# Performance work log

Hardware: AMD Instinct MI355X
Metric: run time of the kernel (lower is better)

The kernel has to match this reference:

```python
import jax, jax.numpy as jnp
import numpy as np

N = 100000
E = 1600000
EMB = 64
IN = 64
HID = 64
HEADS = 3
NEG_SLOPE = 0.2            # PyG GATConv default LeakyReLU slope
RRELU_SLOPE = (1.0 / 8.0 + 1.0 / 3.0) / 2.0  # torch.rrelu eval-mode slope


def setup_inputs() -> dict:
    key = jax.random.key(0)
    ks = jax.random.split(key, 16)
    d_in = IN + EMB
    inp = {
        "z": jax.random.normal(ks[0], (N, EMB), jnp.float32),
        "x": jax.random.normal(ks[1], (N, IN), jnp.float32),
        "edge_index": jax.random.randint(ks[2], (2, E), 0, N, jnp.int32),
        # gat1: (in+emb) -> hidden, 3 heads, concat=False
        "W1": jax.random.normal(ks[3], (d_in, HEADS * HID), jnp.float32) / np.sqrt(d_in),
        "att_src1": jax.random.normal(ks[4], (HEADS, HID), jnp.float32) / np.sqrt(HID),
        "att_dst1": jax.random.normal(ks[5], (HEADS, HID), jnp.float32) / np.sqrt(HID),
        "bias1": jnp.zeros((HID,), jnp.float32),
        # gat2: hidden -> hidden, 3 heads, concat=True
        "W2": jax.random.normal(ks[6], (HID, HEADS * HID), jnp.float32) / np.sqrt(HID),
        "att_src2": jax.random.normal(ks[7], (HEADS, HID), jnp.float32) / np.sqrt(HID),
        "att_dst2": jax.random.normal(ks[8], (HEADS, HID), jnp.float32) / np.sqrt(HID),
        "bias2": jnp.zeros((HEADS * HID,), jnp.float32),
        # final linear hidden*3 -> 1 (with bias)
        "lin_w": jax.random.normal(ks[9], (HEADS * HID, 1), jnp.float32) / np.sqrt(HEADS * HID),
        "lin_b": jnp.zeros((1,), jnp.float32),
    }
    return inp


def rrelu_eval(x):
    return jnp.where(x >= 0, x, x * RRELU_SLOPE)


def gat_conv(x, src, dst, W, a_src, a_dst, bias, concat):
    """PyG GATConv (shared src/dst projection, self-loops already appended)."""
    n = x.shape[0]
    H, C = a_src.shape
    xl = (x @ W).reshape(n, H, C)                       # [N, H, C]
    s = jnp.einsum('nhc,hc->nh', xl, a_src)             # alpha_src per node
    d = jnp.einsum('nhc,hc->nh', xl, a_dst)             # alpha_dst per node
    alpha = jax.nn.leaky_relu(s[src] + d[dst], NEG_SLOPE)  # [E', H]
    amax = jax.ops.segment_max(alpha, dst, num_segments=n)
    ex = jnp.exp(alpha - amax[dst])
    denom = jax.ops.segment_sum(ex, dst, num_segments=n)
    w = ex / (denom[dst] + 1e-16)                       # segment softmax
    out = jax.ops.segment_sum(xl[src] * w[:, :, None], dst, num_segments=n)  # [N,H,C]
    out = out.reshape(n, H * C) if concat else out.mean(axis=1)
    return out + bias


def reference(z, x, edge_index, W1, att_src1, att_dst1, bias1,
              W2, att_src2, att_dst2, bias2, lin_w, lin_b):
    n = x.shape[0]
    loops = jnp.arange(n, dtype=edge_index.dtype)
    src = jnp.concatenate([edge_index[0], loops])       # add self-loops (PyG default)
    dst = jnp.concatenate([edge_index[1], loops])
    h = jnp.concatenate([z, x], axis=1)
    h = rrelu_eval(gat_conv(h, src, dst, W1, att_src1, att_dst1, bias1, concat=False))
    h = rrelu_eval(gat_conv(h, src, dst, W2, att_src2, att_dst2, bias2, concat=True))
    return h @ lin_w + lin_b
```

## Files before the change

### kernel.cpp

```cpp
#include <hip/hip_runtime.h>
#include <cstdint>
#include <cstddef>

#define NEG_SLOPE 0.2f
#define RRELU_SLOPE 0.22916666666666666f

#define BSHIFT 6
#define BCAP 1536
#define MAXNB 1600

typedef _Float16 half4 __attribute__((ext_vector_type(4)));
typedef _Float16 half8 __attribute__((ext_vector_type(8)));
typedef float f32x4 __attribute__((ext_vector_type(4)));

__device__ __forceinline__ float wave_sum64(float v) {
#pragma unroll
  for (int o = 32; o > 0; o >>= 1) v += __shfl_xor(v, o, 64);
  return v;
}

__global__ __launch_bounds__(256) void bucketA(const int* __restrict__ src,
                                               const int* __restrict__ dst, int E, int NB,
                                               int* __restrict__ cursor,
                                               int* __restrict__ region) {
  __shared__ int hist[MAXNB];
  __shared__ int gbase[MAXNB];
  const int tid = threadIdx.x;
  const int chunk = (E + gridDim.x - 1) / gridDim.x;
  const int e0 = blockIdx.x * chunk;
  const int e1 = min(e0 + chunk, E);
  for (int b = tid; b < NB; b += 256) hist[b] = 0;
  __syncthreads();
  for (int i = e0 + tid; i < e1; i += 256) {
    atomicAdd(&hist[dst[i] >> BSHIFT], 1);
  }
  __syncthreads();
  for (int b = tid; b < NB; b += 256) {
    int c = hist[b];
    gbase[b] = (c > 0) ? atomicAdd(&cursor[b], c) : 0;
    hist[b] = 0;
  }
  __syncthreads();
  for (int i = e0 + tid; i < e1; i += 256) {
    int d = dst[i];
    int b = d >> BSHIFT;
    int idx = atomicAdd(&hist[b], 1) + gbase[b];
    if (idx < BCAP) region[b * BCAP + idx] = src[i] | ((d & 63) << 17);
  }
}

__global__ __launch_bounds__(256) void bucket_scan(const int* __restrict__ cursor, int NB,
                                                   int* __restrict__ colbase) {
  __shared__ int lds[256];
  const int tid = threadIdx.x;
  const int K = (NB + 255) / 256;
  int vals[8];
  int s = 0;
#pragma unroll
  for (int j = 0; j < 8; j++) {
    int b = tid * K + j;
    int v = (j < K && b < NB) ? (min(cursor[b], BCAP) + 64) : 0;
    vals[j] = v;
    s += v;
  }
  lds[tid] = s;
  __syncthreads();
  for (int o = 1; o < 256; o <<= 1) {
    int t = (tid >= o) ? lds[tid - o] : 0;
    __syncthreads();
    lds[tid] += t;
    __syncthreads();
  }
  int off = (tid > 0) ? lds[tid - 1] : 0;
#pragma unroll
  for (int j = 0; j < 8; j++) {
    int b = tid * K + j;
    if (j < K && b < NB) colbase[b] = off;
    off += vals[j];
  }
}

__global__ __launch_bounds__(256) void bucketB(const int* __restrict__ region,
                                               const int* __restrict__ cursor,
                                               const int* __restrict__ colbase, int NB,
                                               int* __restrict__ rp, int* __restrict__ col) {
  __shared__ int lcnt[64];
  __shared__ int loff[64];
  const int b = blockIdx.x;
  const int tid = threadIdx.x;
  const int cnt = min(cursor[b], BCAP);
  const int base = colbase[b];
  if (tid < 64) lcnt[tid] = 0;
  __syncthreads();
  const int* reg = region + (size_t)b * BCAP;
  for (int i = tid; i < cnt; i += 256) {
    atomicAdd(&lcnt[reg[i] >> 17], 1);
  }
  __syncthreads();
  if (tid < 64) {
    int v = lcnt[tid] + 1;
    int inc = v;
#pragma unroll
    for (int o = 1; o < 64; o <<= 1) {
      int t = __shfl_up(inc, o, 64);
      if (tid >= o) inc += t;
    }
    int excl = inc - v;
    loff[tid] = excl;
    int n = (b << BSHIFT) + tid;
    rp[n] = base + excl;
    col[base + excl] = n;
    lcnt[tid] = 1;
  }
  __syncthreads();
  for (int i = tid; i < cnt; i += 256) {
    int r = reg[i];
    int ld = r >> 17;
    int idx = atomicAdd(&lcnt[ld], 1);
    col[base + loff[ld] + idx] = r & 0x1FFFF;
  }
}

#define APAD 72
#define BTPAD 72

template <int KC>
__global__ __launch_bounds__(256, 4) void gemm_sd_kernel(
    const float* __restrict__ A0, const float* __restrict__ A1,
    const float* __restrict__ W, const float* __restrict__ asrc,
    const float* __restrict__ adst, _Float16* __restrict__ xlh,
    float* __restrict__ sdS, float* __restrict__ sdD, int N) {
  __shared__ _Float16 A16[64 * APAD];
  __shared__ _Float16 Bt[192 * BTPAD];
  const int tid = threadIdx.x;
  const int w = tid >> 6;
  const int lane = tid & 63;
  const int m = lane & 15;
  const int q = lane >> 4;
  const int m0 = blockIdx.x * 64;

  f32x4 acc[12];
#pragma unroll
  for (int t = 0; t < 12; t++) acc[t] = (f32x4)(0.f);

  for (int kc = 0; kc < KC; kc++) {
    const float* __restrict__ Ab = (KC == 2 && kc == 1) ? A1 : A0;
    if (kc > 0) __syncthreads();
#pragma unroll
    for (int i = 0; i < 4; i++) {
      int f = tid + 256 * i;
      int row = f >> 4;
      int c4 = f & 15;
      int gr = m0 + row;
      gr = (gr < N) ? gr : (N - 1);
      float4 v = *(const float4*)(Ab + (size_t)gr * 64 + c4 * 4);
      half4 hv;
      hv.x = (_Float16)v.x; hv.y = (_Float16)v.y;
      hv.z = (_Float16)v.z; hv.w = (_Float16)v.w;
      *(half4*)&A16[row * APAD + c4 * 4] = hv;
    }
#pragma unroll
    for (int i = 0; i < 6; i++) {
      int f = tid + 256 * i;
      int kg = f / 192;
      int c = f % 192;
      half8 hv;
#pragma unroll
      for (int j = 0; j < 8; j++) {
        hv[j] = (_Float16)W[(size_t)(kc * 64 + kg * 8 + j) * 192 + c];
      }
      *(half8*)&Bt[c * BTPAD + kg * 8] = hv;
    }
    __syncthreads();

#pragma unroll
    for (int t = 0; t < 2; t++) {
      half8 af = *(const half8*)&A16[(w * 16 + m) * APAD + t * 32 + q * 8];
#pragma unroll
      for (int ct = 0; ct < 12; ct++) {
        half8 bf = *(const half8*)&Bt[(ct * 16 + m) * BTPAD + t * 32 + q * 8];
        acc[ct] = __builtin_amdgcn_mfma_f32_16x16x32_f16(af, bf, acc[ct], 0, 0, 0);
      }
    }
  }

  float avs[12], avd[12];
#pragma unroll
  for (int ct = 0; ct < 12; ct++) {
    avs[ct] = asrc[ct * 16 + m];
    avd[ct] = adst[ct * 16 + m];
  }
#pragma unroll
  for (int r = 0; r < 4; r++) {
    const int gr = m0 + w * 16 + q * 4 + r;
    const bool ok = gr < N;
    if (ok) {
#pragma unroll
      for (int ct = 0; ct < 12; ct++) {
        xlh[(size_t)gr * 192 + ct * 16 + m] = (_Float16)acc[ct][r];
      }
    }
#pragma unroll
    for (int h = 0; h < 3; h++) {
      float ps = acc[h * 4 + 0][r] * avs[h * 4 + 0] + acc[h * 4 + 1][r] * avs[h * 4 + 1] +
                 acc[h * 4 + 2][r] * avs[h * 4 + 2] + acc[h * 4 + 3][r] * avs[h * 4 + 3];
      float pd = acc[h * 4 + 0][r] * avd[h * 4 + 0] + acc[h * 4 + 1][r] * avd[h * 4 + 1] +
                 acc[h * 4 + 2][r] * avd[h * 4 + 2] + acc[h * 4 + 3][r] * avd[h * 4 + 3];
#pragma unroll
      for (int o = 1; o < 16; o <<= 1) {
        ps += __shfl_xor(ps, o, 64);
        pd += __shfl_xor(pd, o, 64);
      }
      if (ok && m == 0) {
        sdS[(size_t)gr * 4 + h] = ps;
        sdD[(size_t)gr * 4 + h] = pd;
      }
    }
  }
}

template <int D>
__device__ __forceinline__ void gather_fma_d(const _Float16* __restrict__ xlh,
                                             const float2* __restrict__ wob, int t,
                                             unsigned laneoff, float* acc) {
  half8 xv[D];
  float wgt[D];
#pragma unroll
  for (int u = 0; u < D; u++) {
    float2 rec = wob[2 * (t + u)];
    unsigned off = __float_as_uint(rec.x) + laneoff;
    wgt[u] = rec.y;
    xv[u] = *(const half8*)((const char*)xlh + off);
  }
#pragma unroll
  for (int u = 0; u < D; u++) {
#pragma unroll
    for (int k = 0; k < 8; k++) acc[k] += (float)xv[u][k] * wgt[u];
  }
}

template <int MODE>
__global__ __launch_bounds__(256) void agg_kernel(
    const _Float16* __restrict__ xlh, const float4* __restrict__ sdS,
    const float4* __restrict__ sdD, const int* __restrict__ rp,
    const int* __restrict__ col, const float* __restrict__ bias,
    const float* __restrict__ lw, const float* __restrict__ lb,
    float* __restrict__ out, int N) {
  __shared__ float2 wo[4][3][64];
  const int lane = threadIdx.x & 63;
  const int wv = threadIdx.x >> 6;
  const int n = blockIdx.x * 4 + wv;
  if (n >= N) return;
  const int beg = rp[n], end = rp[n + 1];
  const float4 dd = sdD[n];
  const int s = lane & 31;
  const int h = (s < 24) ? (s >> 3) : 0;
  const int g = s & 7;
  const int par = lane >> 5;
  const unsigned laneoff = (unsigned)(h * 128 + g * 16);
  const float2* wob = &wo[wv][h][par];

  float l0 = 0.f, l1 = 0.f, l2 = 0.f;
  float acc[8];
#pragma unroll
  for (int k = 0; k < 8; k++) acc[k] = 0.f;

  for (int j0 = beg; j0 < end; j0 += 64) {
    const int cntc = min(64, end - j0);
    const bool valid = lane < cntc;
    int srcv = valid ? col[j0 + lane] : 0;
    float4 s4 = sdS[srcv];
    float t0 = s4.x + dd.x, t1 = s4.y + dd.y, t2 = s4.z + dd.z;
    t0 = (t0 < 0.f) ? t0 * NEG_SLOPE : t0;
    t1 = (t1 < 0.f) ? t1 * NEG_SLOPE : t1;
    t2 = (t2 < 0.f) ? t2 * NEG_SLOPE : t2;
    float e0 = valid ? __expf(t0) : 0.f;
    float e1 = valid ? __expf(t1) : 0.f;
    float e2 = valid ? __expf(t2) : 0.f;
    l0 += e0; l1 += e1; l2 += e2;
    const float offb = __uint_as_float((unsigned)srcv * 384u);
    wo[wv][0][lane] = make_float2(offb, e0);
    wo[wv][1][lane] = make_float2(offb, e1);
    wo[wv][2][lane] = make_float2(offb, e2);
    const int steps = (cntc + 1) >> 1;
    int t = 0;
    for (; t + 6 <= steps; t += 6) {
      gather_fma_d<6>(xlh, wob, t, laneoff, acc);
    }
    if (t + 3 <= steps) {
      gather_fma_d<3>(xlh, wob, t, laneoff, acc);
      t += 3;
    }
    if (t + 2 <= steps) {
      gather_fma_d<2>(xlh, wob, t, laneoff, acc);
      t += 2;
    }
    if (t < steps) {
      gather_fma_d<1>(xlh, wob, t, laneoff, acc);
    }
  }

#pragma unroll
  for (int k = 0; k < 8; k++) acc[k] += __shfl_xor(acc[k], 32, 64);
  l0 = wave_sum64(l0);
  l1 = wave_sum64(l1);
  l2 = wave_sum64(l2);
  const float invl = 1.0f / (((h == 0) ? l0 : ((h == 1) ? l1 : l2)) + 1e-16f);
  float v[8];
#pragma unroll
  for (int k = 0; k < 8; k++) v[k] = acc[k] * invl;

  if (MODE == 1) {
    float m[8];
#pragma unroll
    for (int k = 0; k < 8; k++) {
      float a0 = __shfl(v[k], g, 64);
      float a1 = __shfl(v[k], g + 8, 64);
      float a2 = __shfl(v[k], g + 16, 64);
      m[k] = (a0 + a1 + a2) * (1.f / 3.f);
    }
    if (lane < 8) {
      float4 b0 = *(const float4*)(bias + g * 8);
      float4 b1 = *(const float4*)(bias + g * 8 + 4);
      float4 r0, r1;
      r0.x = m[0] + b0.x; r0.y = m[1] + b0.y; r0.z = m[2] + b0.z; r0.w = m[3] + b0.w;
      r1.x = m[4] + b1.x; r1.y = m[5] + b1.y; r1.z = m[6] + b1.z; r1.w = m[7] + b1.w;
      r0.x = (r0.x < 0.f) ? r0.x * RRELU_SLOPE : r0.x;
      r0.y = (r0.y < 0.f) ? r0.y * RRELU_SLOPE : r0.y;
      r0.z = (r0.z < 0.f) ? r0.z * RRELU_SLOPE : r0.z;
      r0.w = (r0.w < 0.f) ? r0.w * RRELU_SLOPE : r0.w;
      r1.x = (r1.x < 0.f) ? r1.x * RRELU_SLOPE : r1.x;
      r1.y = (r1.y < 0.f) ? r1.y * RRELU_SLOPE : r1.y;
      r1.z = (r1.z < 0.f) ? r1.z * RRELU_SLOPE : r1.z;
      r1.w = (r1.w < 0.f) ? r1.w * RRELU_SLOPE : r1.w;
      *(float4*)(out + (size_t)n * 64 + g * 8) = r0;
      *(float4*)(out + (size_t)n * 64 + g * 8 + 4) = r1;
    }
  } else {
    float part = 0.f;
    if (lane < 24) {
      const int c0 = h * 64 + g * 8;
      float4 b0 = *(const float4*)(bias + c0);
      float4 b1 = *(const float4*)(bias + c0 + 4);
      float4 w0 = *(const float4*)(lw + c0);
      float4 w1 = *(const float4*)(lw + c0 + 4);
      float r;
      r = v[0] + b0.x; r = (r < 0.f) ? r * RRELU_SLOPE : r; part += r * w0.x;
      r = v[1] + b0.y; r = (r < 0.f) ? r * RRELU_SLOPE : r; part += r * w0.y;
      r = v[2] + b0.z; r = (r < 0.f) ? r * RRELU_SLOPE : r; part += r * w0.z;
      r = v[3] + b0.w; r = (r < 0.f) ? r * RRELU_SLOPE : r; part += r * w0.w;
      r = v[4] + b1.x; r = (r < 0.f) ? r * RRELU_SLOPE : r; part += r * w1.x;
      r = v[5] + b1.y; r = (r < 0.f) ? r * RRELU_SLOPE : r; part += r * w1.y;
      r = v[6] + b1.z; r = (r < 0.f) ? r * RRELU_SLOPE : r; part += r * w1.z;
      r = v[7] + b1.w; r = (r < 0.f) ? r * RRELU_SLOPE : r; part += r * w1.w;
    }
    part = wave_sum64(part);
    if (lane == 0) out[n] = part + lb[0];
  }
}

extern "C" void kernel_launch(void* const* d_in, const int* in_sizes, int n_in,
                              void* d_out, int out_size, void* d_ws, size_t ws_size,
                              hipStream_t stream) {
  const float* z   = (const float*)d_in[0];
  const float* x   = (const float*)d_in[1];
  const int*   ei  = (const int*)d_in[2];
  const float* W1  = (const float*)d_in[3];
  const float* as1 = (const float*)d_in[4];
  const float* ad1 = (const float*)d_in[5];
  const float* b1  = (const float*)d_in[6];
  const float* W2  = (const float*)d_in[7];
  const float* as2 = (const float*)d_in[8];
  const float* ad2 = (const float*)d_in[9];
  const float* b2  = (const float*)d_in[10];
  const float* lw  = (const float*)d_in[11];
  const float* lb  = (const float*)d_in[12];
  float* out = (float*)d_out;

  const int N = in_sizes[0] / 64;
  const int E = in_sizes[2] / 2;
  const int* srcA = ei;
  const int* dstA = ei + E;
  const int NB = (N + 63) >> BSHIFT;

  char* ws = (char*)d_ws;
  size_t off = 0;
  auto alloc = [&](size_t bytes) -> void* {
    void* p = ws + off;
    off = (off + bytes + 255) & ~(size_t)255;
    return p;
  };
  _Float16* xlh = (_Float16*)alloc((size_t)N * 192 * 2);
  float* h1  = (float*)alloc((size_t)N * 64 * 4);
  float* sdS = (float*)alloc((size_t)N * 4 * 4);
  float* sdD = (float*)alloc((size_t)N * 4 * 4);
  int* region  = (int*)alloc((size_t)NB * BCAP * 4);
  int* cursor  = (int*)alloc((size_t)NB * 4);
  int* colbase = (int*)alloc((size_t)NB * 4);
  int* rp      = (int*)alloc(((size_t)NB * 64 + 1) * 4);
  int* col     = (int*)alloc(((size_t)E + (size_t)NB * 64) * 4);
  if (off > ws_size) return;

  hipMemsetAsync(cursor, 0, (size_t)NB * 4, stream);
  bucketA<<<128, 256, 0, stream>>>(srcA, dstA, E, NB, cursor, region);
  bucket_scan<<<1, 256, 0, stream>>>(cursor, NB, colbase);
  bucketB<<<NB, 256, 0, stream>>>(region, cursor, colbase, NB, rp, col);

  dim3 gg((N + 63) / 64);
  gemm_sd_kernel<2><<<gg, 256, 0, stream>>>(z, x, W1, as1, ad1, xlh, sdS, sdD, N);
  agg_kernel<1><<<(N + 3) / 4, 256, 0, stream>>>(xlh, (const float4*)sdS, (const float4*)sdD,
                                                 rp, col, b1, nullptr, nullptr, h1, N);
  gemm_sd_kernel<1><<<gg, 256, 0, stream>>>(h1, nullptr, W2, as2, ad2, xlh, sdS, sdD, N);
  agg_kernel<2><<<(N + 3) / 4, 256, 0, stream>>>(xlh, (const float4*)sdS, (const float4*)sdD,
                                                 rp, col, b2, lw, lb, out, N);
}
```

Baseline: 449.0 us.

## Fuse edge bucketing pass into first GEMM launch as extra blocks

Merges the bucketA edge-binning kernel with the first-layer projection GEMM into one launch. The first 128 blocks do bucketing and the rest do GEMM tiles, using dynamic shared memory. The aim is to overlap the independent bucketing and GEMM work and save a launch. It also pads the per-wave weight/offset shared buffer in the aggregation kernel from 64 to 68, probably to reduce LDS bank conflicts. The fused kernel uses the GEMM's launch bounds and the larger LDS footprint for every block, which may lower occupancy for the bucketing blocks.

After: 427.4 us. 4.8% less time.

```diff
diff --git a/kernel.cpp b/kernel.cpp
--- a/kernel.cpp
+++ b/kernel.cpp
@@ -9,6 +9,8 @@
 #define BCAP 1536
 #define MAXNB 1600
 
+#define WON 68
+
 typedef _Float16 half4 __attribute__((ext_vector_type(4)));
 typedef _Float16 half8 __attribute__((ext_vector_type(8)));
 typedef float f32x4 __attribute__((ext_vector_type(4)));
@@ -19,15 +21,16 @@
   return v;
 }
 
-__global__ __launch_bounds__(256) void bucketA(const int* __restrict__ src,
-                                               const int* __restrict__ dst, int E, int NB,
-                                               int* __restrict__ cursor,
-                                               int* __restrict__ region) {
-  __shared__ int hist[MAXNB];
-  __shared__ int gbase[MAXNB];
+__device__ __forceinline__ void bucketA_body(char* smem, int bid, int nblk,
+                                             const int* __restrict__ src,
+                                             const int* __restrict__ dst, int E, int NB,
+                                             int* __restrict__ cursor,
+                                             int* __restrict__ region) {
+  int* hist = (int*)smem;
+  int* gbase = hist + MAXNB;
   const int tid = threadIdx.x;
-  const int chunk = (E + gridDim.x - 1) / gridDim.x;
-  const int e0 = blockIdx.x * chunk;
+  const int chunk = (E + nblk - 1) / nblk;
+  const int e0 = bid * chunk;
   const int e1 = min(e0 + chunk, E);
   for (int b = tid; b < NB; b += 256) hist[b] = 0;
   __syncthreads();
@@ -123,21 +126,22 @@
 
 #define APAD 72
 #define BTPAD 72
+#define GEMM_LDS (64 * APAD * 2 + 192 * BTPAD * 2)
 
 template <int KC>
-__global__ __launch_bounds__(256, 4) void gemm_sd_kernel(
+__device__ __forceinline__ void gemm_body(char* smem, int bid,
     const float* __restrict__ A0, const float* __restrict__ A1,
     const float* __restrict__ W, const float* __restrict__ asrc,
     const float* __restrict__ adst, _Float16* __restrict__ xlh,
     float* __restrict__ sdS, float* __restrict__ sdD, int N) {
-  __shared__ _Float16 A16[64 * APAD];
-  __shared__ _Float16 Bt[192 * BTPAD];
+  _Float16* A16 = (_Float16*)smem;
+  _Float16* Bt = A16 + 64 * APAD;
   const int tid = threadIdx.x;
   const int w = tid >> 6;
   const int lane = tid & 63;
   const int m = lane & 15;
   const int q = lane >> 4;
-  const int m0 = blockIdx.x * 64;
+  const int m0 = bid * 64;
 
   f32x4 acc[12];
 #pragma unroll
@@ -219,6 +223,22 @@
   }
 }
 
+template <int KC>
+__global__ __launch_bounds__(256, 4) void gemm_bucketA_fused(
+    const float* __restrict__ A0, const float* __restrict__ A1,
+    const float* __restrict__ W, const float* __restrict__ asrc,
+    const float* __restrict__ adst, _Float16* __restrict__ xlh,
+    float* __restrict__ sdS, float* __restrict__ sdD, int N,
+    const int* __restrict__ src, const int* __restrict__ dst, int E, int NB,
+    int* __restrict__ cursor, int* __restrict__ region, int NBA) {
+  extern __shared__ char smem[];
+  if ((int)blockIdx.x < NBA) {
+    bucketA_body(smem, blockIdx.x, NBA, src, dst, E, NB, cursor, region);
+  } else {
+    gemm_body<KC>(smem, blockIdx.x - NBA, A0, A1, W, asrc, adst, xlh, sdS, sdD, N);
+  }
+}
+
 template <int D>
 __device__ __forceinline__ void gather_fma_d(const _Float16* __restrict__ xlh,
                                              const float2* __restrict__ wob, int t,
@@ -246,7 +266,7 @@
     const int* __restrict__ col, const float* __restrict__ bias,
     const float* __restrict__ lw, const float* __restrict__ lb,
     float* __restrict__ out, int N) {
-  __shared__ float2 wo[4][3][64];
+  __shared__ float2 wo[4][3][WON];
   const int lane = threadIdx.x & 63;
   const int wv = threadIdx.x >> 6;
   const int n = blockIdx.x * 4 + wv;
@@ -382,6 +402,7 @@
   const int* srcA = ei;
   const int* dstA = ei + E;
   const int NB = (N + 63) >> BSHIFT;
+  const int NBA = 128;
 
   char* ws = (char*)d_ws;
   size_t off = 0;
@@ -402,15 +423,17 @@
   if (off > ws_size) return;
 
   hipMemsetAsync(cursor, 0, (size_t)NB * 4, stream);
-  bucketA<<<128, 256, 0, stream>>>(srcA, dstA, E, NB, cursor, region);
+
+  const int gg = (N + 63) / 64;
+  gemm_bucketA_fused<2><<<NBA + gg, 256, GEMM_LDS, stream>>>(
+      z, x, W1, as1, ad1, xlh, sdS, sdD, N, srcA, dstA, E, NB, cursor, region, NBA);
   bucket_scan<<<1, 256, 0, stream>>>(cursor, NB, colbase);
   bucketB<<<NB, 256, 0, stream>>>(region, cursor, colbase, NB, rp, col);
 
-  dim3 gg((N + 63) / 64);
-  gemm_sd_kernel<2><<<gg, 256, 0, stream>>>(z, x, W1, as1, ad1, xlh, sdS, sdD, N);
   agg_kernel<1><<<(N + 3) / 4, 256, 0, stream>>>(xlh, (const float4*)sdS, (const float4*)sdD,
                                                  rp, col, b1, nullptr, nullptr, h1, N);
-  gemm_sd_kernel<1><<<gg, 256, 0, stream>>>(h1, nullptr, W2, as2, ad2, xlh, sdS, sdD, N);
+  gemm_bucketA_fused<1><<<gg, 256, GEMM_LDS, stream>>>(
+      h1, nullptr, W2, as2, ad2, xlh, sdS, sdD, N, nullptr, nullptr, 0, NB, nullptr, nullptr, 0);
   agg_kernel<2><<<(N + 3) / 4, 256, 0, stream>>>(xlh, (const float4*)sdS, (const float4*)sdD,
                                                  rp, col, b2, lw, lb, out, N);
 }
```
